# Performance work log

Hardware: AMD Instinct MI355X
Metric: run time of the kernel (lower is better)

Reference implementation:

```python
import jax, jax.numpy as jnp
import numpy as np

EPS = 1e-7  # keras backend epsilon
B, H, W, C = 16, 112, 112, 64
F, KS = 128, 3


def _stack3x3_same(image):
    # Faithful to SharpCosSim2D.stack3x3 with padding='same', stride=1:
    # zero-padded im2col, kernel offsets row-major, stacked on axis=3.
    b, h, w, c = image.shape
    pimg = jnp.pad(image, ((0, 0), (1, 1), (1, 1), (0, 0)))
    patches = jnp.stack(
        [pimg[:, di:di + h, dj:dj + w, :] for di in range(3) for dj in range(3)],
        axis=3,
    )  # (B, oy, ox, 9, C)
    return patches


def setup_inputs() -> dict:
    key = jax.random.key(0)
    k1, k2 = jax.random.split(key)
    image = jax.random.normal(k1, (B, H, W, C), jnp.float32)
    # glorot-ish scale for the kernel matrix (1, C*k^2, F)
    w = jax.random.normal(k2, (1, C * KS * KS, F), jnp.float32) * (1.0 / np.sqrt(C * KS * KS))
    b_ = jnp.zeros((F,), jnp.float32)   # bias_initializer='zeros'
    p = jnp.ones((F,), jnp.float32)     # sharpening exponent, init ones
    q = jnp.zeros((1,), jnp.float32)    # norm offset, init zeros
    return {"image": image, "w": w, "b": b_, "p": p, "q": q}


def reference(image, w, b, p, q):
    bsz, h, wd, c = image.shape
    x = _stack3x3_same(image)                       # (B, oy, ox, 9, C)
    oy, ox = x.shape[1], x.shape[2]
    x = x.reshape(bsz, oy * ox, KS * KS * c)        # (B, flat, 9*C)
    # l2_normal: sqrt(max(sum_sq, eps)); q^2 added as learnable norm offset
    x_norm = jnp.sqrt(jnp.maximum(jnp.sum(x * x, axis=2, keepdims=True), EPS)) + q * q
    w_norm = jnp.sqrt(jnp.maximum(jnp.sum(w * w, axis=1, keepdims=True), EPS))
    y = jnp.einsum('bnk,ukf->bnf', x / x_norm, w / w_norm)  # cosine sims (B, flat, F)
    sgn = jnp.sign(y)
    y = sgn * jnp.power(jnp.abs(y) + EPS, p * p) + b        # sharpen + bias
    return y.reshape(bsz, oy, ox, F)
```

## Files before the change

kernel.cpp:

```cpp
#include <hip/hip_runtime.h>
#include <hip/hip_bf16.h>

#define EPS 1e-7f

typedef __attribute__((ext_vector_type(8))) short short8;
typedef __attribute__((ext_vector_type(4))) float f32x4;

__device__ __forceinline__ short f2bf(float x) {
    __hip_bfloat16 h = __float2bfloat16(x);
    short r; __builtin_memcpy(&r, &h, 2); return r;
}

__device__ __forceinline__ float fast_log2(float x) {
    float r; asm("v_log_f32 %0, %1" : "=v"(r) : "v"(x)); return r;
}
__device__ __forceinline__ float fast_exp2(float x) {
    float r; asm("v_exp_f32 %0, %1" : "=v"(r) : "v"(x)); return r;
}

__global__ void prep_kernel(const float* __restrict__ w, const float* __restrict__ p,
                            short* __restrict__ Wn, float* __restrict__ p2) {
    __shared__ float pn[4][128];
    __shared__ float sInv[128];
    const int t = blockIdx.x;
    const int tid = threadIdx.x;
    const int n = tid & 127, part = tid >> 7;
    float ssq = 0.f;
    const int k0 = part * 144;
    for (int k = k0; k < k0 + 144; ++k) {
        float v = w[k * 128 + n];
        ssq = fmaf(v, v, ssq);
    }
    pn[part][n] = ssq;
    __syncthreads();
    if (tid < 128) {
        float s = pn[0][tid] + pn[1][tid] + pn[2][tid] + pn[3][tid];
        sInv[tid] = 1.0f / sqrtf(fmaxf(s, EPS));
        if (t == 0) p2[tid] = p[tid] * p[tid];
    }
    __syncthreads();
    if (tid < 256) {
        const int nn = tid & 127, kh = tid >> 7;
        const float inv = sInv[nn];
        short* dst = Wn + t * 8192 + nn * 64 + kh * 32;
        const float* src = w + (t * 64 + kh * 32) * 128 + nn;
#pragma unroll
        for (int j = 0; j < 32; ++j) dst[j] = f2bf(src[j * 128] * inv);
    }
}

__global__ __launch_bounds__(512, 4)
void sharp_main(const float* __restrict__ img, const short* __restrict__ Wn,
                const float* __restrict__ bias, const float* __restrict__ p2g,
                const float* __restrict__ qp, float* __restrict__ out) {
    __shared__ __align__(16) unsigned char lds_img[41472];
    __shared__ __align__(16) unsigned char lds_w[2][16384];
    __shared__ float sArr[324];
    __shared__ float invxn[256];

    const int tid  = threadIdx.x;
    const int lane = tid & 63;
    const int wv   = tid >> 6;
    const int wm   = wv >> 1;
    const int wn   = wv & 1;
    const int tx = blockIdx.x, ty = blockIdx.y, bz = blockIdx.z;
    const int y0 = ty * 16, x0 = tx * 16;

    const int mxl = lane & 15;
    const int kq  = lane >> 4;

    if (tid < 324) sArr[tid] = 0.f;
    __syncthreads();

    {
        const long ibase = (long)bz * (112 * 112 * 64);
        for (int q = tid; q < 2592; q += 512) {
            const int pp = q >> 3, c8 = q & 7;
            const int py = pp / 18, px = pp % 18;
            const int gy = y0 - 1 + py, gx = x0 - 1 + px;
            short8 h = {0, 0, 0, 0, 0, 0, 0, 0};
            if ((unsigned)gy < 112u && (unsigned)gx < 112u) {
                const float* sp = img + ibase + ((gy * 112 + gx) << 6) + (c8 << 3);
                const float4 v0 = *reinterpret_cast<const float4*>(sp);
                const float4 v1 = *reinterpret_cast<const float4*>(sp + 4);
                float ss = v0.x * v0.x + v0.y * v0.y + v0.z * v0.z + v0.w * v0.w
                         + v1.x * v1.x + v1.y * v1.y + v1.z * v1.z + v1.w * v1.w;
                h[0] = f2bf(v0.x); h[1] = f2bf(v0.y); h[2] = f2bf(v0.z); h[3] = f2bf(v0.w);
                h[4] = f2bf(v1.x); h[5] = f2bf(v1.y); h[6] = f2bf(v1.z); h[7] = f2bf(v1.w);
                atomicAdd(&sArr[pp], ss);
            }
            const int addr = (pp << 7) + (((c8 << 4)) ^ ((pp & 7) << 4));
            *reinterpret_cast<short8*>(lds_img + addr) = h;
        }
    }

    const uint4* wg = reinterpret_cast<const uint4*>(Wn);
    const int wi0 = tid * 2, wi1 = tid * 2 + 1;
    const int wa0 = (tid * 32) ^ ((((tid * 32) >> 7) & 7) << 4);
    const int wa1 = (tid * 32 + 16) ^ ((((tid * 32) >> 7) & 7) << 4);
    uint4 r0 = wg[wi0], r1 = wg[wi1];
    *reinterpret_cast<uint4*>(lds_w[0] + wa0) = r0;
    *reinterpret_cast<uint4*>(lds_w[0] + wa1) = r1;
    r0 = wg[1024 + wi0]; r1 = wg[1024 + wi1];

    __syncthreads();

    if (tid < 256) {
        const int my = tid >> 4, mx = tid & 15;
        float s9 = 0.f;
#pragma unroll
        for (int dy = 0; dy < 3; ++dy)
#pragma unroll
            for (int dx = 0; dx < 3; ++dx)
                s9 += sArr[(my + dy) * 18 + (mx + dx)];
        const float qv = qp[0];
        invxn[tid] = 1.0f / (sqrtf(fmaxf(s9, EPS)) + qv * qv);
    }
    __syncthreads();

    f32x4 acc[4][4];
#pragma unroll
    for (int mi = 0; mi < 4; ++mi)
#pragma unroll
        for (int ni = 0; ni < 4; ++ni)
            acc[mi][ni] = (f32x4){0.f, 0.f, 0.f, 0.f};

#pragma unroll
    for (int t = 0; t < 9; ++t) {
        const int dy = t / 3, dx = t % 3;
        if (t < 8) {
            *reinterpret_cast<uint4*>(lds_w[(t + 1) & 1] + wa0) = r0;
            *reinterpret_cast<uint4*>(lds_w[(t + 1) & 1] + wa1) = r1;
            if (t < 7) { r0 = wg[(t + 2) * 1024 + wi0]; r1 = wg[(t + 2) * 1024 + wi1]; }
        }
#pragma unroll
        for (int ks = 0; ks < 2; ++ks) {
            short8 wf[4], af[4];
#pragma unroll
            for (int ni = 0; ni < 4; ++ni) {
                const int nn = wn * 64 + ni * 16 + mxl;
                const int addr = (nn << 7) + ((ks * 64 + kq * 16) ^ ((nn & 7) << 4));
                wf[ni] = *reinterpret_cast<const short8*>(lds_w[t & 1] + addr);
            }
#pragma unroll
            for (int mi = 0; mi < 4; ++mi) {
                const int pp = (wm * 4 + mi + dy) * 18 + mxl + dx;
                const int addr = (pp << 7) + ((ks * 64 + kq * 16) ^ ((pp & 7) << 4));
                af[mi] = *reinterpret_cast<const short8*>(lds_img + addr);
            }
#pragma unroll
            for (int mi = 0; mi < 4; ++mi)
#pragma unroll
                for (int ni = 0; ni < 4; ++ni)
                    acc[mi][ni] = __builtin_amdgcn_mfma_f32_16x16x32_bf16(
                        wf[ni], af[mi], acc[mi][ni], 0, 0, 0);
        }
        __syncthreads();
    }

    f32x4 p2v[4], bv[4];
#pragma unroll
    for (int ni = 0; ni < 4; ++ni) {
        const int f0 = wn * 64 + ni * 16 + kq * 4;
        p2v[ni] = *reinterpret_cast<const f32x4*>(p2g + f0);
        bv[ni]  = *reinterpret_cast<const f32x4*>(bias + f0);
    }
    const long obase = (long)bz * 112 * 112 * 128;
#pragma unroll
    for (int mi = 0; mi < 4; ++mi) {
        const int my = wm * 4 + mi;
        const int gy = y0 + my;
        const float inv = invxn[my * 16 + mxl];
        float* op = out + obase + ((long)(gy * 112 + x0 + mxl) << 7);
#pragma unroll
        for (int ni = 0; ni < 4; ++ni) {
            f32x4 v;
#pragma unroll
            for (int j = 0; j < 4; ++j) {
                const float cosv = acc[mi][ni][j] * inv;
                const float av = fabsf(cosv) + EPS;
                const float r = fast_exp2(p2v[ni][j] * fast_log2(av));
                v[j] = (cosv == 0.f) ? bv[ni][j] : (copysignf(r, cosv) + bv[ni][j]);
            }
            *reinterpret_cast<f32x4*>(op + wn * 64 + ni * 16 + kq * 4) = v;
        }
    }
}

extern "C" void kernel_launch(void* const* d_in, const int* in_sizes, int n_in,
                              void* d_out, int out_size, void* d_ws, size_t ws_size,
                              hipStream_t stream) {
    const float* img = (const float*)d_in[0];
    const float* w   = (const float*)d_in[1];
    const float* b   = (const float*)d_in[2];
    const float* p   = (const float*)d_in[3];
    const float* q   = (const float*)d_in[4];
    float* out = (float*)d_out;

    short* Wn = (short*)d_ws;
    float* p2 = (float*)((char*)d_ws + 9 * 8192 * 2);

    prep_kernel<<<9, 512, 0, stream>>>(w, p, Wn, p2);
    sharp_main<<<dim3(7, 7, 16), 512, 0, stream>>>(img, Wn, b, p2, q, out);
}
```

Baseline: 226.5 us.

## Swizzle block order, shuffle-reduce norms, and stage output through LDS

Flattens the grid and remaps block IDs so that each group of blocks (likely per XCD) handles contiguous tiles for better L2 locality. Replaces LDS atomic accumulation of pixel sum-of-squares with a wave shuffle reduction and drops the zero-init barrier. Stages each wave's epilogue results through swizzled LDS scratch so global stores write wider contiguous row segments. This adds extra LDS traffic and relies on per-wave lockstep for the reused scratch region.

Result: faster. 218.7 us (-3.5%).

```diff
diff --git a/kernel.cpp b/kernel.cpp
--- a/kernel.cpp
+++ b/kernel.cpp
@@ -63,14 +63,16 @@
     const int wv   = tid >> 6;
     const int wm   = wv >> 1;
     const int wn   = wv & 1;
-    const int tx = blockIdx.x, ty = blockIdx.y, bz = blockIdx.z;
+
+    const int bid  = blockIdx.x;
+    const int work = (bid & 7) * 98 + (bid >> 3);
+    const int bz = work / 49;
+    const int rem = work - bz * 49;
+    const int ty = rem / 7, tx = rem - ty * 7;
     const int y0 = ty * 16, x0 = tx * 16;
 
     const int mxl = lane & 15;
     const int kq  = lane >> 4;
-
-    if (tid < 324) sArr[tid] = 0.f;
-    __syncthreads();
 
     {
         const long ibase = (long)bz * (112 * 112 * 64);
@@ -79,16 +81,20 @@
             const int py = pp / 18, px = pp % 18;
             const int gy = y0 - 1 + py, gx = x0 - 1 + px;
             short8 h = {0, 0, 0, 0, 0, 0, 0, 0};
+            float ss = 0.f;
             if ((unsigned)gy < 112u && (unsigned)gx < 112u) {
                 const float* sp = img + ibase + ((gy * 112 + gx) << 6) + (c8 << 3);
                 const float4 v0 = *reinterpret_cast<const float4*>(sp);
                 const float4 v1 = *reinterpret_cast<const float4*>(sp + 4);
-                float ss = v0.x * v0.x + v0.y * v0.y + v0.z * v0.z + v0.w * v0.w
-                         + v1.x * v1.x + v1.y * v1.y + v1.z * v1.z + v1.w * v1.w;
+                ss = v0.x * v0.x + v0.y * v0.y + v0.z * v0.z + v0.w * v0.w
+                   + v1.x * v1.x + v1.y * v1.y + v1.z * v1.z + v1.w * v1.w;
                 h[0] = f2bf(v0.x); h[1] = f2bf(v0.y); h[2] = f2bf(v0.z); h[3] = f2bf(v0.w);
                 h[4] = f2bf(v1.x); h[5] = f2bf(v1.y); h[6] = f2bf(v1.z); h[7] = f2bf(v1.w);
-                atomicAdd(&sArr[pp], ss);
-            }
+            }
+            ss += __shfl_xor(ss, 1);
+            ss += __shfl_xor(ss, 2);
+            ss += __shfl_xor(ss, 4);
+            if ((q & 7) == 0) sArr[pp] = ss;
             const int addr = (pp << 7) + (((c8 << 4)) ^ ((pp & 7) << 4));
             *reinterpret_cast<short8*>(lds_img + addr) = h;
         }
@@ -166,12 +172,12 @@
         bv[ni]  = *reinterpret_cast<const f32x4*>(bias + f0);
     }
     const long obase = (long)bz * 112 * 112 * 128;
+    unsigned char* scratch = lds_img + (wv << 12);
 #pragma unroll
     for (int mi = 0; mi < 4; ++mi) {
         const int my = wm * 4 + mi;
         const int gy = y0 + my;
         const float inv = invxn[my * 16 + mxl];
-        float* op = out + obase + ((long)(gy * 112 + x0 + mxl) << 7);
 #pragma unroll
         for (int ni = 0; ni < 4; ++ni) {
             f32x4 v;
@@ -182,7 +188,16 @@
                 const float r = fast_exp2(p2v[ni][j] * fast_log2(av));
                 v[j] = (cosv == 0.f) ? bv[ni][j] : (copysignf(r, cosv) + bv[ni][j]);
             }
-            *reinterpret_cast<f32x4*>(op + wn * 64 + ni * 16 + kq * 4) = v;
+            const int wb = (mxl * 256 + ni * 64 + kq * 16) ^ ((mxl & 7) << 4);
+            *reinterpret_cast<f32x4*>(scratch + wb) = v;
+        }
+#pragma unroll
+        for (int it = 0; it < 4; ++it) {
+            const int p = it * 4 + kq;
+            const int rb = (p * 256 + mxl * 16) ^ ((p & 7) << 4);
+            const f32x4 v = *reinterpret_cast<const f32x4*>(scratch + rb);
+            float* op = out + obase + ((long)(gy * 112 + x0 + p) << 7) + wn * 64 + mxl * 4;
+            *reinterpret_cast<f32x4*>(op) = v;
         }
     }
 }
@@ -201,5 +216,5 @@
     float* p2 = (float*)((char*)d_ws + 9 * 8192 * 2);
 
     prep_kernel<<<9, 512, 0, stream>>>(w, p, Wn, p2);
-    sharp_main<<<dim3(7, 7, 16), 512, 0, stream>>>(img, Wn, b, p2, q, out);
-}
+    sharp_main<<<784, 512, 0, stream>>>(img, Wn, b, p2, q, out);
+}
```
